# Optimization experiments

Measured on AMD Instinct MI355X. Metric: run time of the kernel, lower is better.

The kernel has to match this reference:

```python
import jax, jax.numpy as jnp
import numpy as np

N = 64   # SSM state size
H = 256  # channels
B = 8    # batch
L = 1024 # sequence length


def setup_inputs() -> dict:
    key = jax.random.key(0)
    k1, k2, k3, k4, k5 = jax.random.split(key, 5)
    scale = 1.0 / np.sqrt(N)  # lecun_normal std for fan_in=N
    inp = jax.random.normal(k1, (B, L, H), jnp.float32)
    As = jax.random.normal(k2, (H, N, N), jnp.float32) * scale
    Bs = jax.random.normal(k3, (H, N, 1), jnp.float32) * scale
    Cs = jax.random.normal(k4, (H, 1, N), jnp.float32) * scale
    Ds = jnp.ones((H,), jnp.float32)
    # log_step_initializer: uniform in [log(dt_min), log(dt_max)]
    lo, hi = np.log(0.001), np.log(0.003)
    log_steps = jax.random.uniform(k5, (H,), jnp.float32) * (hi - lo) + lo
    return {"inp": inp, "As": As, "Bs": Bs, "Cs": Cs, "Ds": Ds, "log_steps": log_steps}


def _discretize(A, B_, C, step):
    # Bilinear (Tustin) discretization, batched over H. step: (H,)
    I = jnp.eye(A.shape[-1], dtype=A.dtype)
    s = (step / 2.0)[:, None, None]            # (H,1,1)
    lhs = I - s * A                            # (H,N,N)
    Ab = jnp.linalg.solve(lhs, I + s * A)      # (H,N,N)
    Bb = jnp.linalg.solve(lhs, (2.0 * s) * B_) # (H,N,1)
    return Ab, Bb, C


def _kernel(Ab, Bb, Cb, length):
    # K[l] = Cb @ Ab^l @ Bb, built via a scan over matrix powers (all heads batched)
    def body(x, _):
        k = jnp.einsum('hon,hno->h', Cb, x)          # (H,)
        x_next = jnp.einsum('hmn,hno->hmo', Ab, x)   # (H,N,1)
        return x_next, k
    _, K = jax.lax.scan(body, Bb, None, length=length)
    return K  # (L, H)


def reference(inp, As, Bs, Cs, Ds, log_steps):
    Lseq = inp.shape[1]
    step = jnp.exp(log_steps)
    Ab, Bb, Cb = _discretize(As, Bs, Cs, step)
    K = _kernel(Ab, Bb, Cb, Lseq)                      # (L, H)
    # causal (non-circular) convolution via FFT, per channel
    n = 2 * Lseq
    Uf = jnp.fft.rfft(inp, n=n, axis=1)                # (B, F, H)
    Kf = jnp.fft.rfft(K, n=n, axis=0)[None]            # (1, F, H)
    y = jnp.fft.irfft(Uf * Kf, n=n, axis=1)[:, :Lseq]  # (B, L, H)
    return y + Ds[None, None, :] * inp
```

## Files before the change

### kernel.cpp

```cpp
#include <hip/hip_runtime.h>
#include <cstddef>

#define SSM_N 64
#define SSM_H 256
#define SSM_B 8
#define SSM_L 1024
#define PADM  68
#define PADC  68
#define KTP   1040

__global__ __launch_bounds__(256) void ssm_prep_kernel(
    const float* __restrict__ As, const float* __restrict__ Bsin,
    const float* __restrict__ Csin, const float* __restrict__ logsteps,
    float* __restrict__ KTout)
{
    __shared__ __align__(16) float B0[SSM_N * PADM];
    __shared__ __align__(16) float B1[SSM_N * PADM];
    __shared__ __align__(16) float CallL[32 * PADC];
    __shared__ __align__(16) float XallL[32 * PADC];
    __shared__ float pbuf[4 * 64];

    const int h    = blockIdx.x;
    const int tid  = threadIdx.x;
    const int lane = tid & 63;
    const int q    = tid >> 6;
    const int j0   = q * 16;

    const float step = expf(logsteps[h]);
    const float s    = 0.5f * step;

    float arow[64];
    {
        const float4* Ar = reinterpret_cast<const float4*>(As + (size_t)h * 4096 + lane * 64);
        #pragma unroll
        for (int r = 0; r < 16; ++r) {
            float4 v = Ar[r];
            arow[4*r+0] = s * v.x; arow[4*r+1] = s * v.y;
            arow[4*r+2] = s * v.z; arow[4*r+3] = s * v.w;
        }
        if (q == 0) {
            float4* wp = reinterpret_cast<float4*>(B1 + lane * PADM);
            #pragma unroll
            for (int r = 0; r < 16; ++r)
                wp[r] = make_float4(arow[4*r], arow[4*r+1], arow[4*r+2], arow[4*r+3]);
        }
    }
    __syncthreads();

    #pragma unroll 1
    for (int it = 0; it < 2; ++it) {
        const float* Bop = (it == 0) ? B1 : B0;
        float acc[16];
        #pragma unroll
        for (int jj = 0; jj < 16; ++jj) acc[jj] = arow[j0 + jj];
        #pragma unroll
        for (int k = 0; k < 64; ++k) {
            const float a = arow[k];
            const float4* bp = reinterpret_cast<const float4*>(Bop + k * PADM + j0);
            const float4 b0 = bp[0], b1v = bp[1], b2 = bp[2], b3 = bp[3];
            acc[0]  += a * b0.x;  acc[1]  += a * b0.y;  acc[2]  += a * b0.z;  acc[3]  += a * b0.w;
            acc[4]  += a * b1v.x; acc[5]  += a * b1v.y; acc[6]  += a * b1v.z; acc[7]  += a * b1v.w;
            acc[8]  += a * b2.x;  acc[9]  += a * b2.y;  acc[10] += a * b2.z;  acc[11] += a * b2.w;
            acc[12] += a * b3.x;  acc[13] += a * b3.y;  acc[14] += a * b3.z;  acc[15] += a * b3.w;
        }
        float4* wp = reinterpret_cast<float4*>(B0 + lane * PADM + j0);
        wp[0] = make_float4(acc[0],  acc[1],  acc[2],  acc[3]);
        wp[1] = make_float4(acc[4],  acc[5],  acc[6],  acc[7]);
        wp[2] = make_float4(acc[8],  acc[9],  acc[10], acc[11]);
        wp[3] = make_float4(acc[12], acc[13], acc[14], acc[15]);
    }
    __syncthreads();

    if (q == 0)      pbuf[lane]  = Bsin[h * SSM_N + lane];
    else if (q == 1) CallL[lane] = Csin[h * SSM_N + lane];
    #pragma unroll
    for (int r = 0; r < 16; ++r) {
        int e = r * 256 + tid, i = e >> 6, j = e & 63;
        B1[j * PADM + i] = 2.f * B0[i * PADM + j] + ((i == j) ? 1.f : 0.f);
    }
    __syncthreads();

    if (q == 0) {
        float accb = 0.f;
        #pragma unroll
        for (int r = 0; r < 16; ++r) {
            const float4 sv = *reinterpret_cast<const float4*>(B0 + lane * PADM + 4 * r);
            accb += sv.x * pbuf[4*r] + sv.y * pbuf[4*r+1] + sv.z * pbuf[4*r+2] + sv.w * pbuf[4*r+3];
        }
        XallL[lane] = step * (pbuf[lane] + accb);
    }

    #pragma unroll 1
    for (int j = 0; j < 31; ++j) {
        const float* crow = CallL + j * PADC;
        float pp = 0.f;
        #pragma unroll
        for (int r = 0; r < 4; ++r) {
            const float4 cc = *reinterpret_cast<const float4*>(crow + j0 + 4 * r);
            const float4 aa = *reinterpret_cast<const float4*>(B1 + lane * PADM + j0 + 4 * r);
            pp += cc.x * aa.x + cc.y * aa.y + cc.z * aa.z + cc.w * aa.w;
        }
        pbuf[q * 64 + lane] = pp;
        __syncthreads();
        if (q == 0)
            CallL[(j + 1) * PADC + lane] =
                pbuf[lane] + pbuf[64 + lane] + pbuf[128 + lane] + pbuf[192 + lane];
        __syncthreads();
    }

    {
        float* src = B1;
        float* dst = B0;
        #pragma unroll 1
        for (int it = 0; it < 5; ++it) {
            #pragma unroll
            for (int r = 0; r < 16; ++r) {
                const float4 v = *reinterpret_cast<const float4*>(src + lane * PADM + 4 * r);
                arow[4*r] = v.x; arow[4*r+1] = v.y; arow[4*r+2] = v.z; arow[4*r+3] = v.w;
            }
            float acc[16];
            #pragma unroll
            for (int jj = 0; jj < 16; ++jj) acc[jj] = 0.f;
            #pragma unroll
            for (int k = 0; k < 64; ++k) {
                const float a = arow[k];
                const float4* bp = reinterpret_cast<const float4*>(src + k * PADM + j0);
                const float4 b0 = bp[0], b1v = bp[1], b2 = bp[2], b3 = bp[3];
                acc[0]  += a * b0.x;  acc[1]  += a * b0.y;  acc[2]  += a * b0.z;  acc[3]  += a * b0.w;
                acc[4]  += a * b1v.x; acc[5]  += a * b1v.y; acc[6]  += a * b1v.z; acc[7]  += a * b1v.w;
                acc[8]  += a * b2.x;  acc[9]  += a * b2.y;  acc[10] += a * b2.z;  acc[11] += a * b2.w;
                acc[12] += a * b3.x;  acc[13] += a * b3.y;  acc[14] += a * b3.z;  acc[15] += a * b3.w;
            }
            float4* wp = reinterpret_cast<float4*>(dst + lane * PADM + j0);
            wp[0] = make_float4(acc[0],  acc[1],  acc[2],  acc[3]);
            wp[1] = make_float4(acc[4],  acc[5],  acc[6],  acc[7]);
            wp[2] = make_float4(acc[8],  acc[9],  acc[10], acc[11]);
            wp[3] = make_float4(acc[12], acc[13], acc[14], acc[15]);
            __syncthreads();
            float* tmp = src; src = dst; dst = tmp;
        }
    }

    #pragma unroll
    for (int r = 0; r < 16; ++r) {
        int e = r * 256 + tid, i = e >> 6, jj = e & 63;
        B1[i * PADM + jj] = B0[jj * PADM + i];
    }
    __syncthreads();

    #pragma unroll 1
    for (int m = 0; m < 31; ++m) {
        const float* xrow = XallL + m * PADC;
        float pp = 0.f;
        #pragma unroll
        for (int r = 0; r < 4; ++r) {
            const float4 xx = *reinterpret_cast<const float4*>(xrow + j0 + 4 * r);
            const float4 aa = *reinterpret_cast<const float4*>(B1 + lane * PADM + j0 + 4 * r);
            pp += xx.x * aa.x + xx.y * aa.y + xx.z * aa.z + xx.w * aa.w;
        }
        pbuf[q * 64 + lane] = pp;
        __syncthreads();
        if (q == 0)
            XallL[(m + 1) * PADC + lane] =
                pbuf[lane] + pbuf[64 + lane] + pbuf[128 + lane] + pbuf[192 + lane];
        __syncthreads();
    }

    #pragma unroll
    for (int r = 0; r < 4; ++r) {
        int l = r * 256 + tid, mm = l >> 5, jj = l & 31;
        const float4* cr = reinterpret_cast<const float4*>(CallL + jj * PADC);
        const float4* xr = reinterpret_cast<const float4*>(XallL + mm * PADC);
        float sacc = 0.f;
        #pragma unroll
        for (int i = 0; i < 16; ++i) {
            const float4 c4 = cr[i], x4 = xr[i];
            sacc += c4.x * x4.x + c4.y * x4.y + c4.z * x4.z + c4.w * x4.w;
        }
        KTout[(size_t)h * KTP + l] = sacc;
    }
}

__global__ __launch_bounds__(256) void ssm_ktr_kernel(
    const float* __restrict__ KT, float* __restrict__ K)
{
    __shared__ float tile[32][33];
    const int l0 = (blockIdx.x & 31) * 32;
    const int h0 = (blockIdx.x >> 5) * 32;
    const int c  = threadIdx.x & 31;
    const int r0 = threadIdx.x >> 5;
    #pragma unroll
    for (int k = 0; k < 4; ++k)
        tile[r0 + 8 * k][c] = KT[(size_t)(h0 + r0 + 8 * k) * KTP + l0 + c];
    __syncthreads();
    #pragma unroll
    for (int k = 0; k < 4; ++k)
        K[(size_t)(l0 + r0 + 8 * k) * SSM_H + h0 + c] = tile[c][r0 + 8 * k];
}

__global__ __launch_bounds__(256) void ssm_conv_kernel(
    const float* __restrict__ U, const float* __restrict__ Kk,
    const float* __restrict__ Ds, float* __restrict__ Y)
{
    const int h = threadIdx.x;
    const int b = blockIdx.x & 7;
    const int p = blockIdx.x >> 3;
    const float dh = Ds[h];
    const float* Ub = U + (size_t)b * SSM_L * SSM_H + h;
    float* Yb = Y + (size_t)b * SSM_L * SSM_H + h;

    #pragma unroll
    for (int half = 0; half < 2; ++half) {
        const int t  = (half == 0) ? p : (127 - p);
        const int l0 = t << 3;
        float acc[8], win[15], kreg[8], u0[8];

        #pragma unroll
        for (int j = 0; j < 15; ++j) {
            const int li = l0 - 7 + j;
            win[j] = (li >= 0) ? Ub[li * SSM_H] : 0.f;
        }
        #pragma unroll
        for (int i = 0; i < 8; ++i) { acc[i] = 0.f; u0[i] = win[7 + i]; }
        #pragma unroll
        for (int j = 0; j < 8; ++j) kreg[j] = Kk[j * SSM_H + h];

        const float* kp = Kk + 8 * SSM_H + h;
        const float* up = Ub + (l0 - 15) * SSM_H;
        #pragma unroll 2
        for (int c = 0; c < t - 1; ++c) {
            float kn[8], nw[8];
            #pragma unroll
            for (int j = 0; j < 8; ++j) kn[j] = kp[j * SSM_H];
            #pragma unroll
            for (int j = 0; j < 8; ++j) nw[j] = up[j * SSM_H];
            #pragma unroll
            for (int dd = 0; dd < 8; ++dd) {
                const float kv = kreg[dd];
                #pragma unroll
                for (int i = 0; i < 8; ++i) acc[i] += kv * win[7 + i - dd];
            }
            #pragma unroll
            for (int j = 14; j >= 8; --j) win[j] = win[j - 8];
            #pragma unroll
            for (int j = 0; j < 8; ++j) { win[j] = nw[j]; kreg[j] = kn[j]; }
            kp += 8 * SSM_H;
            up -= 8 * SSM_H;
        }

        if (t >= 1) {
            float kn[8];
            #pragma unroll
            for (int j = 0; j < 8; ++j) kn[j] = Kk[(8 * t + j) * SSM_H + h];
            const float uz = Ub[0];
            #pragma unroll
            for (int dd = 0; dd < 8; ++dd) {
                const float kv = kreg[dd];
                #pragma unroll
                for (int i = 0; i < 8; ++i) acc[i] += kv * win[7 + i - dd];
            }
            #pragma unroll
            for (int j = 14; j >= 8; --j) win[j] = win[j - 8];
            #pragma unroll
            for (int j = 0; j < 7; ++j) win[j] = 0.f;
            win[7] = uz;
            #pragma unroll
            for (int j = 0; j < 8; ++j) kreg[j] = kn[j];
        }

        #pragma unroll
        for (int dd = 0; dd < 8; ++dd) {
            const float kv = kreg[dd];
            #pragma unroll
            for (int i = 0; i < 8; ++i) acc[i] += kv * win[7 + i - dd];
        }

        #pragma unroll
        for (int i = 0; i < 8; ++i)
            Yb[(l0 + i) * SSM_H] = acc[i] + dh * u0[i];
    }
}

extern "C" void kernel_launch(void* const* d_in, const int* in_sizes, int n_in,
                              void* d_out, int out_size, void* d_ws, size_t ws_size,
                              hipStream_t stream)
{
    const float* inp    = (const float*)d_in[0];
    const float* As     = (const float*)d_in[1];
    const float* Bsin   = (const float*)d_in[2];
    const float* Csin   = (const float*)d_in[3];
    const float* Dsin   = (const float*)d_in[4];
    const float* lsteps = (const float*)d_in[5];
    float* Y    = (float*)d_out;
    float* KT   = (float*)d_out;
    float* Kbuf = (float*)d_ws;

    ssm_prep_kernel<<<dim3(SSM_H), dim3(256), 0, stream>>>(As, Bsin, Csin, lsteps, KT);
    ssm_ktr_kernel<<<dim3(256), dim3(256), 0, stream>>>(KT, Kbuf);
    ssm_conv_kernel<<<dim3(SSM_B * 64), dim3(256), 0, stream>>>(inp, Kbuf, Dsin, Y);
}
```

Baseline: 197.2 us.

## Use register-tiled 4x4 matmuls and doubling for power tables; enlarge conv register tile

The prep kernel now runs its dense 64x64 matmuls with a 4x4-per-thread register tile read from shared memory, in place of one-row-per-thread with a 64-float register array. The two 31-step sequential vector-matrix chains that built the C and X power tables are replaced by log-depth doubling that reuses the repeated matrix squarings. This removes most of the per-step barriers and reductions. The direct causal convolution kernel moves from an 8-output to a 16-output register window with 128-thread blocks, giving more reuse per loaded element at the cost of more registers and possibly lower occupancy.

```diff
diff --git a/kernel.cpp b/kernel.cpp
--- a/kernel.cpp
+++ b/kernel.cpp
@@ -6,171 +6,195 @@
 #define SSM_B 8
 #define SSM_L 1024
 #define PADM  68
-#define PADC  68
 #define KTP   1040
+
+__device__ __forceinline__ void mm_tile(const float* __restrict__ A,
+                                        const float* __restrict__ B,
+                                        int ti, int tj, float acc[4][4])
+{
+    #pragma unroll
+    for (int kb = 0; kb < 16; ++kb) {
+        float4 av[4], bv4[4];
+        #pragma unroll
+        for (int ii = 0; ii < 4; ++ii)
+            av[ii] = *reinterpret_cast<const float4*>(A + (4*ti+ii)*PADM + 4*kb);
+        #pragma unroll
+        for (int kk = 0; kk < 4; ++kk)
+            bv4[kk] = *reinterpret_cast<const float4*>(B + (4*kb+kk)*PADM + 4*tj);
+        #pragma unroll
+        for (int kk = 0; kk < 4; ++kk) {
+            const float b0 = bv4[kk].x, b1 = bv4[kk].y, b2 = bv4[kk].z, b3 = bv4[kk].w;
+            #pragma unroll
+            for (int ii = 0; ii < 4; ++ii) {
+                const float a = reinterpret_cast<const float*>(&av[ii])[kk];
+                acc[ii][0] += a * b0; acc[ii][1] += a * b1;
+                acc[ii][2] += a * b2; acc[ii][3] += a * b3;
+            }
+        }
+    }
+}
 
 __global__ __launch_bounds__(256) void ssm_prep_kernel(
     const float* __restrict__ As, const float* __restrict__ Bsin,
     const float* __restrict__ Csin, const float* __restrict__ logsteps,
     float* __restrict__ KTout)
 {
-    __shared__ __align__(16) float B0[SSM_N * PADM];
-    __shared__ __align__(16) float B1[SSM_N * PADM];
-    __shared__ __align__(16) float CallL[32 * PADC];
-    __shared__ __align__(16) float XallL[32 * PADC];
-    __shared__ float pbuf[4 * 64];
+    __shared__ __align__(16) float Ea[SSM_N * PADM];
+    __shared__ __align__(16) float Eb[SSM_N * PADM];
+    __shared__ __align__(16) float Cm[32 * PADM];
+    __shared__ __align__(16) float Xm[32 * PADM];
+    __shared__ float bvs[64];
 
     const int h    = blockIdx.x;
     const int tid  = threadIdx.x;
     const int lane = tid & 63;
     const int q    = tid >> 6;
-    const int j0   = q * 16;
+    const int ti   = tid & 15;
+    const int tj   = tid >> 4;
 
     const float step = expf(logsteps[h]);
     const float s    = 0.5f * step;
 
-    float arow[64];
+    float breg = 0.f, creg = 0.f;
+    if (q == 0) breg = Bsin[h * SSM_N + lane];
+    if (q == 1) creg = Csin[h * SSM_N + lane];
+
+    #pragma unroll
+    for (int r = 0; r < 4; ++r) {
+        float4 v = *reinterpret_cast<const float4*>(As + (size_t)h * 4096 + 1024 * r + 4 * tid);
+        const int i = 16 * r + tj;
+        *reinterpret_cast<float4*>(Ea + i * PADM + 4 * ti) =
+            make_float4(s * v.x, s * v.y, s * v.z, s * v.w);
+    }
+    if (q == 0) bvs[lane] = breg;
+    __syncthreads();
+
     {
-        const float4* Ar = reinterpret_cast<const float4*>(As + (size_t)h * 4096 + lane * 64);
-        #pragma unroll
-        for (int r = 0; r < 16; ++r) {
-            float4 v = Ar[r];
-            arow[4*r+0] = s * v.x; arow[4*r+1] = s * v.y;
-            arow[4*r+2] = s * v.z; arow[4*r+3] = s * v.w;
-        }
-        if (q == 0) {
-            float4* wp = reinterpret_cast<float4*>(B1 + lane * PADM);
-            #pragma unroll
-            for (int r = 0; r < 16; ++r)
-                wp[r] = make_float4(arow[4*r], arow[4*r+1], arow[4*r+2], arow[4*r+3]);
-        }
-    }
-    __syncthreads();
-
-    #pragma unroll 1
-    for (int it = 0; it < 2; ++it) {
-        const float* Bop = (it == 0) ? B1 : B0;
-        float acc[16];
-        #pragma unroll
-        for (int jj = 0; jj < 16; ++jj) acc[jj] = arow[j0 + jj];
-        #pragma unroll
-        for (int k = 0; k < 64; ++k) {
-            const float a = arow[k];
-            const float4* bp = reinterpret_cast<const float4*>(Bop + k * PADM + j0);
-            const float4 b0 = bp[0], b1v = bp[1], b2 = bp[2], b3 = bp[3];
-            acc[0]  += a * b0.x;  acc[1]  += a * b0.y;  acc[2]  += a * b0.z;  acc[3]  += a * b0.w;
-            acc[4]  += a * b1v.x; acc[5]  += a * b1v.y; acc[6]  += a * b1v.z; acc[7]  += a * b1v.w;
-            acc[8]  += a * b2.x;  acc[9]  += a * b2.y;  acc[10] += a * b2.z;  acc[11] += a * b2.w;
-            acc[12] += a * b3.x;  acc[13] += a * b3.y;  acc[14] += a * b3.z;  acc[15] += a * b3.w;
-        }
-        float4* wp = reinterpret_cast<float4*>(B0 + lane * PADM + j0);
-        wp[0] = make_float4(acc[0],  acc[1],  acc[2],  acc[3]);
-        wp[1] = make_float4(acc[4],  acc[5],  acc[6],  acc[7]);
-        wp[2] = make_float4(acc[8],  acc[9],  acc[10], acc[11]);
-        wp[3] = make_float4(acc[12], acc[13], acc[14], acc[15]);
-    }
-    __syncthreads();
-
-    if (q == 0)      pbuf[lane]  = Bsin[h * SSM_N + lane];
-    else if (q == 1) CallL[lane] = Csin[h * SSM_N + lane];
-    #pragma unroll
-    for (int r = 0; r < 16; ++r) {
-        int e = r * 256 + tid, i = e >> 6, j = e & 63;
-        B1[j * PADM + i] = 2.f * B0[i * PADM + j] + ((i == j) ? 1.f : 0.f);
-    }
+        float acc[4][4];
+        #pragma unroll
+        for (int ii = 0; ii < 4; ++ii) {
+            float4 m4 = *reinterpret_cast<const float4*>(Ea + (4*ti+ii)*PADM + 4*tj);
+            acc[ii][0] = m4.x; acc[ii][1] = m4.y; acc[ii][2] = m4.z; acc[ii][3] = m4.w;
+        }
+        mm_tile(Ea, Ea, ti, tj, acc);
+        #pragma unroll
+        for (int ii = 0; ii < 4; ++ii)
+            *reinterpret_cast<float4*>(Eb + (4*ti+ii)*PADM + 4*tj) =
+                make_float4(acc[ii][0], acc[ii][1], acc[ii][2], acc[ii][3]);
+    }
+    __syncthreads();
+
+    {
+        float acc[4][4];
+        #pragma unroll
+        for (int ii = 0; ii < 4; ++ii) {
+            float4 m4 = *reinterpret_cast<const float4*>(Ea + (4*ti+ii)*PADM + 4*tj);
+            acc[ii][0] = m4.x; acc[ii][1] = m4.y; acc[ii][2] = m4.z; acc[ii][3] = m4.w;
+        }
+        mm_tile(Ea, Eb, ti, tj, acc);
+        __syncthreads();
+        #pragma unroll
+        for (int ii = 0; ii < 4; ++ii) {
+            float4 w;
+            w.x = 2.f*acc[ii][0] + ((4*ti+ii) == (4*tj+0) ? 1.f : 0.f);
+            w.y = 2.f*acc[ii][1] + ((4*ti+ii) == (4*tj+1) ? 1.f : 0.f);
+            w.z = 2.f*acc[ii][2] + ((4*ti+ii) == (4*tj+2) ? 1.f : 0.f);
+            w.w = 2.f*acc[ii][3] + ((4*ti+ii) == (4*tj+3) ? 1.f : 0.f);
+            *reinterpret_cast<float4*>(Eb + (4*ti+ii)*PADM + 4*tj) = w;
+        }
+    }
+    if (q == 1) Cm[lane] = creg;
     __syncthreads();
 
     if (q == 0) {
         float accb = 0.f;
         #pragma unroll
         for (int r = 0; r < 16; ++r) {
-            const float4 sv = *reinterpret_cast<const float4*>(B0 + lane * PADM + 4 * r);
-            accb += sv.x * pbuf[4*r] + sv.y * pbuf[4*r+1] + sv.z * pbuf[4*r+2] + sv.w * pbuf[4*r+3];
-        }
-        XallL[lane] = step * (pbuf[lane] + accb);
-    }
-
+            float4 e4 = *reinterpret_cast<const float4*>(Eb + lane * PADM + 4 * r);
+            accb += e4.x * bvs[4*r] + e4.y * bvs[4*r+1] + e4.z * bvs[4*r+2] + e4.w * bvs[4*r+3];
+        }
+        Xm[lane] = s * (accb + bvs[lane]);
+    }
+    __syncthreads();
+
+    float* Ecur = Eb;
+    float* Enext = Ea;
     #pragma unroll 1
-    for (int j = 0; j < 31; ++j) {
-        const float* crow = CallL + j * PADC;
-        float pp = 0.f;
-        #pragma unroll
-        for (int r = 0; r < 4; ++r) {
-            const float4 cc = *reinterpret_cast<const float4*>(crow + j0 + 4 * r);
-            const float4 aa = *reinterpret_cast<const float4*>(B1 + lane * PADM + j0 + 4 * r);
-            pp += cc.x * aa.x + cc.y * aa.y + cc.z * aa.z + cc.w * aa.w;
-        }
-        pbuf[q * 64 + lane] = pp;
+    for (int k = 0; k < 5; ++k) {
+        const int rr = tid >> 4;
+        if (rr < (1 << k)) {
+            const float* crow = Cm + rr * PADM;
+            float a0 = 0.f, a1 = 0.f, a2 = 0.f, a3 = 0.f;
+            #pragma unroll
+            for (int kb = 0; kb < 16; ++kb) {
+                float4 c4 = *reinterpret_cast<const float4*>(crow + 4 * kb);
+                #pragma unroll
+                for (int kk = 0; kk < 4; ++kk) {
+                    float4 e4 = *reinterpret_cast<const float4*>(Ecur + (4*kb+kk)*PADM + 4*ti);
+                    const float cc = reinterpret_cast<const float*>(&c4)[kk];
+                    a0 += cc * e4.x; a1 += cc * e4.y; a2 += cc * e4.z; a3 += cc * e4.w;
+                }
+            }
+            *reinterpret_cast<float4*>(Cm + (rr + (1 << k)) * PADM + 4 * ti) =
+                make_float4(a0, a1, a2, a3);
+        }
+        {
+            float acc[4][4];
+            #pragma unroll
+            for (int ii = 0; ii < 4; ++ii)
+                acc[ii][0] = acc[ii][1] = acc[ii][2] = acc[ii][3] = 0.f;
+            mm_tile(Ecur, Ecur, ti, tj, acc);
+            #pragma unroll
+            for (int ii = 0; ii < 4; ++ii)
+                *reinterpret_cast<float4*>(Enext + (4*ti+ii)*PADM + 4*tj) =
+                    make_float4(acc[ii][0], acc[ii][1], acc[ii][2], acc[ii][3]);
+        }
         __syncthreads();
-        if (q == 0)
-            CallL[(j + 1) * PADC + lane] =
-                pbuf[lane] + pbuf[64 + lane] + pbuf[128 + lane] + pbuf[192 + lane];
+        float* tmp = Ecur; Ecur = Enext; Enext = tmp;
+    }
+
+    #pragma unroll 1
+    for (int k = 0; k < 5; ++k) {
+        const int mm_ = tid >> 4;
+        if (mm_ < (1 << k)) {
+            const float* xrow = Xm + mm_ * PADM;
+            float a0 = 0.f, a1 = 0.f, a2 = 0.f, a3 = 0.f;
+            #pragma unroll
+            for (int kb = 0; kb < 16; ++kb) {
+                float4 x4 = *reinterpret_cast<const float4*>(xrow + 4 * kb);
+                float4 f0 = *reinterpret_cast<const float4*>(Ecur + (4*ti+0)*PADM + 4*kb);
+                float4 f1 = *reinterpret_cast<const float4*>(Ecur + (4*ti+1)*PADM + 4*kb);
+                float4 f2 = *reinterpret_cast<const float4*>(Ecur + (4*ti+2)*PADM + 4*kb);
+                float4 f3 = *reinterpret_cast<const float4*>(Ecur + (4*ti+3)*PADM + 4*kb);
+                a0 += f0.x*x4.x + f0.y*x4.y + f0.z*x4.z + f0.w*x4.w;
+                a1 += f1.x*x4.x + f1.y*x4.y + f1.z*x4.z + f1.w*x4.w;
+                a2 += f2.x*x4.x + f2.y*x4.y + f2.z*x4.z + f2.w*x4.w;
+                a3 += f3.x*x4.x + f3.y*x4.y + f3.z*x4.z + f3.w*x4.w;
+            }
+            *reinterpret_cast<float4*>(Xm + (mm_ + (1 << k)) * PADM + 4 * ti) =
+                make_float4(a0, a1, a2, a3);
+        }
+        if (k < 4) {
+            float acc[4][4];
+            #pragma unroll
+            for (int ii = 0; ii < 4; ++ii)
+                acc[ii][0] = acc[ii][1] = acc[ii][2] = acc[ii][3] = 0.f;
+            mm_tile(Ecur, Ecur, ti, tj, acc);
+            #pragma unroll
+            for (int ii = 0; ii < 4; ++ii)
+                *reinterpret_cast<float4*>(Enext + (4*ti+ii)*PADM + 4*tj) =
+                    make_float4(acc[ii][0], acc[ii][1], acc[ii][2], acc[ii][3]);
+        }
         __syncthreads();
-    }
-
-    {
-        float* src = B1;
-        float* dst = B0;
-        #pragma unroll 1
-        for (int it = 0; it < 5; ++it) {
-            #pragma unroll
-            for (int r = 0; r < 16; ++r) {
-                const float4 v = *reinterpret_cast<const float4*>(src + lane * PADM + 4 * r);
-                arow[4*r] = v.x; arow[4*r+1] = v.y; arow[4*r+2] = v.z; arow[4*r+3] = v.w;
-            }
-            float acc[16];
-            #pragma unroll
-            for (int jj = 0; jj < 16; ++jj) acc[jj] = 0.f;
-            #pragma unroll
-            for (int k = 0; k < 64; ++k) {
-                const float a = arow[k];
-                const float4* bp = reinterpret_cast<const float4*>(src + k * PADM + j0);
-                const float4 b0 = bp[0], b1v = bp[1], b2 = bp[2], b3 = bp[3];
-                acc[0]  += a * b0.x;  acc[1]  += a * b0.y;  acc[2]  += a * b0.z;  acc[3]  += a * b0.w;
-                acc[4]  += a * b1v.x; acc[5]  += a * b1v.y; acc[6]  += a * b1v.z; acc[7]  += a * b1v.w;
-                acc[8]  += a * b2.x;  acc[9]  += a * b2.y;  acc[10] += a * b2.z;  acc[11] += a * b2.w;
-                acc[12] += a * b3.x;  acc[13] += a * b3.y;  acc[14] += a * b3.z;  acc[15] += a * b3.w;
-            }
-            float4* wp = reinterpret_cast<float4*>(dst + lane * PADM + j0);
-            wp[0] = make_float4(acc[0],  acc[1],  acc[2],  acc[3]);
-            wp[1] = make_float4(acc[4],  acc[5],  acc[6],  acc[7]);
-            wp[2] = make_float4(acc[8],  acc[9],  acc[10], acc[11]);
-            wp[3] = make_float4(acc[12], acc[13], acc[14], acc[15]);
-            __syncthreads();
-            float* tmp = src; src = dst; dst = tmp;
-        }
-    }
-
-    #pragma unroll
-    for (int r = 0; r < 16; ++r) {
-        int e = r * 256 + tid, i = e >> 6, jj = e & 63;
-        B1[i * PADM + jj] = B0[jj * PADM + i];
-    }
-    __syncthreads();
-
-    #pragma unroll 1
-    for (int m = 0; m < 31; ++m) {
-        const float* xrow = XallL + m * PADC;
-        float pp = 0.f;
-        #pragma unroll
-        for (int r = 0; r < 4; ++r) {
-            const float4 xx = *reinterpret_cast<const float4*>(xrow + j0 + 4 * r);
-            const float4 aa = *reinterpret_cast<const float4*>(B1 + lane * PADM + j0 + 4 * r);
-            pp += xx.x * aa.x + xx.y * aa.y + xx.z * aa.z + xx.w * aa.w;
-        }
-        pbuf[q * 64 + lane] = pp;
-        __syncthreads();
-        if (q == 0)
-            XallL[(m + 1) * PADC + lane] =
-                pbuf[lane] + pbuf[64 + lane] + pbuf[128 + lane] + pbuf[192 + lane];
-        __syncthreads();
+        float* tmp = Ecur; Ecur = Enext; Enext = tmp;
     }
 
     #pragma unroll
     for (int r = 0; r < 4; ++r) {
-        int l = r * 256 + tid, mm = l >> 5, jj = l & 31;
-        const float4* cr = reinterpret_cast<const float4*>(CallL + jj * PADC);
-        const float4* xr = reinterpret_cast<const float4*>(XallL + mm * PADC);
+        const int l = r * 256 + tid;
+        const int m_ = l >> 5, j_ = l & 31;
+        const float4* cr = reinterpret_cast<const float4*>(Cm + j_ * PADM);
+        const float4* xr = reinterpret_cast<const float4*>(Xm + m_ * PADM);
         float sacc = 0.f;
         #pragma unroll
         for (int i = 0; i < 16; ++i) {
@@ -198,86 +222,92 @@
         K[(size_t)(l0 + r0 + 8 * k) * SSM_H + h0 + c] = tile[c][r0 + 8 * k];
 }
 
-__global__ __launch_bounds__(256) void ssm_conv_kernel(
+__global__ __launch_bounds__(128) void ssm_conv_kernel(
     const float* __restrict__ U, const float* __restrict__ Kk,
     const float* __restrict__ Ds, float* __restrict__ Y)
 {
-    const int h = threadIdx.x;
-    const int b = blockIdx.x & 7;
-    const int p = blockIdx.x >> 3;
+    const int tid = threadIdx.x;
+    const int b   = blockIdx.x & 7;
+    const int pp  = (blockIdx.x >> 3) & 31;
+    const int hg  = blockIdx.x >> 8;
+    const int h   = (hg << 7) + tid;
     const float dh = Ds[h];
     const float* Ub = U + (size_t)b * SSM_L * SSM_H + h;
     float* Yb = Y + (size_t)b * SSM_L * SSM_H + h;
 
     #pragma unroll
     for (int half = 0; half < 2; ++half) {
-        const int t  = (half == 0) ? p : (127 - p);
-        const int l0 = t << 3;
-        float acc[8], win[15], kreg[8], u0[8];
-
-        #pragma unroll
-        for (int j = 0; j < 15; ++j) {
-            const int li = l0 - 7 + j;
-            win[j] = (li >= 0) ? Ub[li * SSM_H] : 0.f;
-        }
-        #pragma unroll
-        for (int i = 0; i < 8; ++i) { acc[i] = 0.f; u0[i] = win[7 + i]; }
-        #pragma unroll
-        for (int j = 0; j < 8; ++j) kreg[j] = Kk[j * SSM_H + h];
-
-        const float* kp = Kk + 8 * SSM_H + h;
-        const float* up = Ub + (l0 - 15) * SSM_H;
-        #pragma unroll 2
+        const int t  = (half == 0) ? pp : (63 - pp);
+        const int l0 = t << 4;
+        float acc[16], win[31], kreg[16];
+        #pragma unroll
+        for (int i = 0; i < 16; ++i) acc[i] = 0.f;
+
+        if (t == 0) {
+            #pragma unroll
+            for (int j = 0; j < 31; ++j)
+                win[j] = (j >= 15) ? Ub[(j - 15) * SSM_H] : 0.f;
+        } else {
+            #pragma unroll
+            for (int j = 0; j < 31; ++j)
+                win[j] = Ub[(l0 - 15 + j) * SSM_H];
+        }
+        #pragma unroll
+        for (int j = 0; j < 16; ++j) kreg[j] = Kk[j * SSM_H + h];
+
+        const float* kp = Kk + 16 * SSM_H + h;
+        const float* up = Ub + (l0 - 31) * SSM_H;
+        #pragma unroll 1
         for (int c = 0; c < t - 1; ++c) {
-            float kn[8], nw[8];
-            #pragma unroll
-            for (int j = 0; j < 8; ++j) kn[j] = kp[j * SSM_H];
-            #pragma unroll
-            for (int j = 0; j < 8; ++j) nw[j] = up[j * SSM_H];
-            #pragma unroll
-            for (int dd = 0; dd < 8; ++dd) {
+            float kn[16], nw[16];
+            #pragma unroll
+            for (int j = 0; j < 16; ++j) kn[j] = kp[j * SSM_H];
+            #pragma unroll
+            for (int j = 0; j < 16; ++j) nw[j] = up[j * SSM_H];
+            #pragma unroll
+            for (int dd = 0; dd < 16; ++dd) {
                 const float kv = kreg[dd];
                 #pragma unroll
-                for (int i = 0; i < 8; ++i) acc[i] += kv * win[7 + i - dd];
-            }
-            #pragma unroll
-            for (int j = 14; j >= 8; --j) win[j] = win[j - 8];
-            #pragma unroll
-            for (int j = 0; j < 8; ++j) { win[j] = nw[j]; kreg[j] = kn[j]; }
-            kp += 8 * SSM_H;
-            up -= 8 * SSM_H;
+                for (int i = 0; i < 16; ++i) acc[i] += kv * win[15 + i - dd];
+            }
+            #pragma unroll
+            for (int j = 30; j >= 16; --j) win[j] = win[j - 16];
+            #pragma unroll
+            for (int j = 0; j < 16; ++j) { win[j] = nw[j]; kreg[j] = kn[j]; }
+            kp += 16 * SSM_H;
+            up -= 16 * SSM_H;
         }
 
         if (t >= 1) {
-            float kn[8];
-            #pragma unroll
-            for (int j = 0; j < 8; ++j) kn[j] = Kk[(8 * t + j) * SSM_H + h];
+            float kn[16];
+            #pragma unroll
+            for (int j = 0; j < 16; ++j) kn[j] = Kk[(16 * t + j) * SSM_H + h];
             const float uz = Ub[0];
             #pragma unroll
-            for (int dd = 0; dd < 8; ++dd) {
+            for (int dd = 0; dd < 16; ++dd) {
                 const float kv = kreg[dd];
                 #pragma unroll
-                for (int i = 0; i < 8; ++i) acc[i] += kv * win[7 + i - dd];
-            }
-            #pragma unroll
-            for (int j = 14; j >= 8; --j) win[j] = win[j - 8];
-            #pragma unroll
-            for (int j = 0; j < 7; ++j) win[j] = 0.f;
-            win[7] = uz;
-            #pragma unroll
-            for (int j = 0; j < 8; ++j) kreg[j] = kn[j];
-        }
-
-        #pragma unroll
-        for (int dd = 0; dd < 8; ++dd) {
+                for (int i = 0; i < 16; ++i) acc[i] += kv * win[15 + i - dd];
+            }
+            #pragma unroll
+            for (int j = 30; j >= 16; --j) win[j] = win[j - 16];
+            #pragma unroll
+            for (int j = 0; j < 15; ++j) win[j] = 0.f;
+            win[15] = uz;
+            #pragma unroll
+            for (int j = 0; j < 16; ++j) kreg[j] = kn[j];
+        }
+
+        #pragma unroll
+        for (int dd = 0; dd < 16; ++dd) {
             const float kv = kreg[dd];
             #pragma unroll
-            for (int i = 0; i < 8; ++i) acc[i] += kv * win[7 + i - dd];
-        }
-
-        #pragma unroll
-        for (int i = 0; i < 8; ++i)
-            Yb[(l0 + i) * SSM_H] = acc[i] + dh * u0[i];
+            for (int i = 0; i < 16; ++i) acc[i] += kv * win[15 + i - dd];
+        }
+
+        #pragma unroll
+        for (int i = 0; i < 16; ++i)
+            Yb[(l0 + i) * SSM_H] = acc[i] + dh * Ub[(l0 + i) * SSM_H];
     }
 }
 
@@ -297,5 +327,5 @@
 
     ssm_prep_kernel<<<dim3(SSM_H), dim3(256), 0, stream>>>(As, Bsin, Csin, lsteps, KT);
     ssm_ktr_kernel<<<dim3(256), dim3(256), 0, stream>>>(KT, Kbuf);
-    ssm_conv_kernel<<<dim3(SSM_B * 64), dim3(256), 0, stream>>>(inp, Kbuf, Dsin, Y);
-}
+    ssm_conv_kernel<<<dim3(512), dim3(128), 0, stream>>>(inp, Kbuf, Dsin, Y);
+}
```

Result: no change. 198.3 us (+0.6%).
